# Kernel optimization log

Measured on AMD Instinct MI355X. Metric: run time of the kernel, lower is better.

The kernel has to match this reference:

```python
import jax, jax.numpy as jnp
import numpy as np

B_SZ, SEQ, H, N, NB = 64, 2048, 256, 256, 2
NUM_ITEMS, NC = 200000, 101
EPS = 1e-5


def _ln(x, g, b):
    m = x.mean(-1, keepdims=True)
    v = ((x - m) ** 2).mean(-1, keepdims=True)
    return (x - m) / jnp.sqrt(v + EPS) * g + b


def _s4(u, log_A_real, A_imag, Bp, Cp, Dp, log_step):
    # u: [B,S,H]; diagonal complex S4 recurrence x_{t} = A_bar*x_{t-1} + B_bar u_t
    step = jnp.exp(log_step)                      # [1]
    A = -jnp.exp(log_A_real) + 1j * A_imag        # [N] complex64
    A_bar = jnp.exp(A * step)                     # [N]
    # faithful to torch broadcast (requires N==H): coef scales hidden axis
    B_bar = ((A_bar - 1.0) / A)[None, :] * Bp     # [N,H] complex
    Cc = Cp[..., 0] + 1j * Cp[..., 1]             # [H,N] complex

    def step_fn(x, u_t):                          # x: [B,N] complex, u_t: [B,H]
        x = A_bar[None, :] * x + (u_t.astype(jnp.complex64) @ B_bar.T)
        y = jnp.real(jnp.einsum('hn,bn->bh', Cc, x)) + Dp[None, :] * u_t
        return x, y

    x0 = jnp.zeros((u.shape[0], N), dtype=jnp.complex64)
    _, ys = jax.lax.scan(step_fn, x0, jnp.swapaxes(u, 0, 1))  # ys: [S,B,H]
    return jnp.swapaxes(ys, 0, 1)


def setup_inputs():
    key = jax.random.key(0)
    ks = jax.random.split(key, 16)
    d = {}
    d['input_seqs'] = jax.random.randint(ks[0], (B_SZ, SEQ), 0, NUM_ITEMS + 1)
    d['item_idxs'] = jax.random.randint(ks[1], (B_SZ, NC), 0, NUM_ITEMS + 1)
    d['item_emb'] = jax.random.normal(ks[2], (NUM_ITEMS + 1, H)) * 0.02
    d['pos_emb'] = jax.random.normal(ks[3], (SEQ, H)) * 0.02
    d['ln_g'] = jnp.ones((NB, H)); d['ln_b'] = jnp.zeros((NB, H))
    d['log_A_real'] = jax.random.normal(ks[4], (NB, N))
    d['A_imag'] = jax.random.normal(ks[5], (NB, N))
    d['B_ssm'] = jax.random.normal(ks[6], (NB, N, H))
    d['C_ssm'] = jax.random.normal(ks[7], (NB, H, N, 2))
    d['D_ssm'] = jax.random.normal(ks[8], (NB, H))
    d['log_step'] = jax.random.normal(ks[9], (NB, 1)) * 0.1
    d['W1'] = jax.random.normal(ks[10], (NB, H, H)) / np.sqrt(H).astype(np.float32)
    d['b1'] = jnp.zeros((NB, H))
    d['W2'] = jax.random.normal(ks[11], (NB, H, H)) / np.sqrt(H).astype(np.float32)
    d['b2'] = jnp.zeros((NB, H))
    d['ln_f_g'] = jnp.ones((H,)); d['ln_f_b'] = jnp.zeros((H,))
    return d


def reference(input_seqs, item_idxs, item_emb, pos_emb, ln_g, ln_b,
              log_A_real, A_imag, B_ssm, C_ssm, D_ssm, log_step,
              W1, b1, W2, b2, ln_f_g, ln_f_b):
    mask = (input_seqs != 0).astype(item_emb.dtype)          # [B,S]
    x = item_emb[input_seqs] + pos_emb[None, :, :]           # [B,S,H]
    x = x * mask[..., None]
    for i in range(NB):
        h = _ln(x, ln_g[i], ln_b[i])
        x = x + _s4(h, log_A_real[i], A_imag[i], B_ssm[i], C_ssm[i], D_ssm[i], log_step[i])
        h2 = _ln(x, ln_g[i], ln_b[i])
        x = x + (jax.nn.relu(h2 @ W1[i] + b1[i]) @ W2[i] + b2[i])
        x = x * mask[..., None]
    x = _ln(x, ln_f_g, ln_f_b)
    cand = item_emb[item_idxs]                               # [B,C,H]
    logits = jnp.einsum('bh,bch->bc', x[:, -1], cand)        # [B,C]
    return logits
```

## Files before the change

kernel.cpp:

```cpp
#include <hip/hip_runtime.h>
#include <hip/hip_bf16.h>

#define BSZ 64
#define SEQ 2048
#define HD  256
#define ND  256
#define BS_TOK (BSZ*SEQ)
#define NCAND 101
#define EPS 1e-5f

using bf16 = __hip_bfloat16;
typedef unsigned short u16;
typedef unsigned int   u32;
typedef __attribute__((ext_vector_type(8))) short short8v;
typedef __attribute__((ext_vector_type(4))) float f32x4;

__device__ __forceinline__ float clampf(float v, float c) { return fminf(fmaxf(v, -c), c); }

__device__ __forceinline__ void split_bf(float x, u16& h, u16& l) {
  u32 u = __float_as_uint(x);
  h = (u16)(u >> 16);
  float d = x - __uint_as_float(u & 0xffff0000u);
  l = (u16)(__float_as_uint(d) >> 16);
}
__device__ __forceinline__ float comb_bf(u16 h, u16 l) {
  return __uint_as_float((u32)h << 16) + __uint_as_float((u32)l << 16);
}

__device__ __forceinline__ void async_copy16(const void* g, void* l) {
  __builtin_amdgcn_global_load_lds(
      (const __attribute__((address_space(1))) void*)g,
      (__attribute__((address_space(3))) void*)l, 16, 0, 0);
}


static constexpr size_t MiB = 1024*1024;
static constexpr size_t OFF_X    = 0;
static constexpr size_t OFF_PR   = 128*MiB;
static constexpr size_t OFF_WB   = OFF_PR + 4096;
static constexpr size_t OFF_XLR  = OFF_WB + 4*MiB;
static constexpr size_t OFF_XLI  = OFF_XLR + 65536;
static constexpr size_t OFF_YL   = OFF_XLI + 65536;
static constexpr size_t OFF_XF   = OFF_YL  + 65536;
static constexpr size_t OFF_CH   = 136*MiB;

static constexpr int WB_BB0H = 0,       WB_BB0L = 131072;
static constexpr int WB_BB1H = 262144,  WB_BB1L = 393216;
static constexpr int WB_WSH  = 524288,  WB_WSL  = 655360;
static constexpr int WB_W1H  = 786432,  WB_W1L  = 851968;
static constexpr int WB_W2H  = 917504,  WB_W2L  = 983040;

__global__ __launch_bounds__(256) void pack_k(
    const float* __restrict__ lar, const float* __restrict__ aim, const float* __restrict__ lstep,
    const float* __restrict__ C0, const float* __restrict__ W1, const float* __restrict__ W2,
    const float* __restrict__ Bf,
    float* __restrict__ pr, u16* __restrict__ wb)
{
  int gid = blockIdx.x*256 + threadIdx.x;
  if (gid < 512) {
    int blk = gid >> 8;
    float step = expf(clampf(lstep[blk], 10.f));
    float ar = -expf(clampf(lar[gid], 20.f));
    float ai = aim[gid];
    float er = expf(fminf(ar*step, 0.f));
    pr[gid]       = er * cosf(ai*step);
    pr[512 + gid] = er * sinf(ai*step);
  }
  int r = gid >> 8, c = gid & 255;
  u16 h, l;
#pragma unroll
  for (int blk = 0; blk < 2; ++blk) {
    float step = expf(clampf(lstep[blk], 10.f));
    float ar = -expf(clampf(lar[blk*256 + c], 20.f));
    float ai = aim[blk*256 + c];
    float er  = expf(fminf(ar*step, 0.f));
    float abr = er * cosf(ai*step);
    float abi = er * sinf(ai*step);
    float den = ar*ar + ai*ai;
    float tr = abr - 1.f, ti = abi;
    float cr = (tr*ar + ti*ai) / den;
    float ci = (ti*ar - tr*ai) / den;
    float bv = Bf[blk*65536 + r*256 + c];
    u16* Bh = wb + (blk ? WB_BB1H : WB_BB0H);
    u16* Bl = wb + (blk ? WB_BB1L : WB_BB0L);
    split_bf(cr * bv, h, l); Bh[r*256 + c] = h;         Bl[r*256 + c] = l;
    split_bf(ci * bv, h, l); Bh[(256+r)*256 + c] = h;   Bl[(256+r)*256 + c] = l;
  }
  split_bf( C0[(size_t)(r*256 + c)*2    ], h, l);
  wb[WB_WSH + r*512 + c] = h;        wb[WB_WSL + r*512 + c] = l;
  split_bf(-C0[(size_t)(r*256 + c)*2 + 1], h, l);
  wb[WB_WSH + r*512 + 256 + c] = h;  wb[WB_WSL + r*512 + 256 + c] = l;
  split_bf(W1[c*256 + r], h, l); wb[WB_W1H + r*256 + c] = h; wb[WB_W1L + r*256 + c] = l;
  split_bf(W2[c*256 + r], h, l); wb[WB_W2H + r*256 + c] = h; wb[WB_W2L + r*256 + c] = l;
}

__device__ __forceinline__ void store4_planes(u16* rowp, int lane, int rb7,
                                              float a, float b, float c, float d) {
  int idx = ((lane >> 4) << 7) + (((((lane & 15) >> 1)) ^ rb7) << 3) + ((lane & 1) << 2);
  u16 h0,l0,h1,l1,h2,l2,h3,l3;
  split_bf(a, h0, l0); split_bf(b, h1, l1); split_bf(c, h2, l2); split_bf(d, h3, l3);
  *(uint2*)(rowp + idx)      = make_uint2((u32)h0 | ((u32)h1 << 16), (u32)h2 | ((u32)h3 << 16));
  *(uint2*)(rowp + idx + 64) = make_uint2((u32)l0 | ((u32)l1 << 16), (u32)l2 | ((u32)l3 << 16));
}

__global__ __launch_bounds__(256) void ln_emb_k(
    const int* __restrict__ seqs, const float* __restrict__ iemb,
    const float* __restrict__ pemb,
    const float* __restrict__ g, const float* __restrict__ b,
    float* __restrict__ Xf, u16* __restrict__ OutP, const float* __restrict__ Dv)
{
  int w = threadIdx.x >> 6, lane = threadIdx.x & 63;
  size_t row = (size_t)blockIdx.x * 4 + w;
  int id = seqs[row];
  int pos = (int)(row & (SEQ-1));
  float x[4] = {0.f, 0.f, 0.f, 0.f};
  if (id != 0) {
    float4 ev = ((const float4*)(iemb + (size_t)id*HD))[lane];
    float4 pv = ((const float4*)(pemb + (size_t)pos*HD))[lane];
    x[0] = ev.x + pv.x; x[1] = ev.y + pv.y; x[2] = ev.z + pv.z; x[3] = ev.w + pv.w;
  }
  float s = 0.f, s2 = 0.f;
#pragma unroll
  for (int k = 0; k < 4; ++k) { s += x[k]; s2 += x[k]*x[k]; }
#pragma unroll
  for (int off = 32; off > 0; off >>= 1) { s += __shfl_xor(s, off, 64); s2 += __shfl_xor(s2, off, 64); }
  float m = s * (1.f/256.f);
  float var = fmaxf(s2 * (1.f/256.f) - m*m, 0.f);
  float rinv = rsqrtf(var + EPS);
  int c0 = lane*4;
  float u[4], nx[4];
#pragma unroll
  for (int k = 0; k < 4; ++k) {
    u[k] = (x[k] - m) * rinv * g[c0+k] + b[c0+k];
    nx[k] = x[k] + Dv[c0+k] * u[k];
  }
  store4_planes(OutP + row*512, lane, (int)(row & 7), u[0], u[1], u[2], u[3]);
  ((float4*)(Xf + row*HD))[lane] = make_float4(nx[0], nx[1], nx[2], nx[3]);
}

__global__ __launch_bounds__(256) void ln_rows(
    float* __restrict__ Xf, const float* __restrict__ g, const float* __restrict__ b,
    u16* __restrict__ OutP)
{
  int w = threadIdx.x >> 6, lane = threadIdx.x & 63;
  size_t row = (size_t)blockIdx.x * 4 + w;
  float* xrow = Xf + row*HD;
  float4 xv = ((const float4*)xrow)[lane];
  float x[4] = {xv.x, xv.y, xv.z, xv.w};
  float s = 0.f, s2 = 0.f;
#pragma unroll
  for (int k = 0; k < 4; ++k) { s += x[k]; s2 += x[k]*x[k]; }
#pragma unroll
  for (int off = 32; off > 0; off >>= 1) { s += __shfl_xor(s, off, 64); s2 += __shfl_xor(s2, off, 64); }
  float m = s * (1.f/256.f);
  float var = fmaxf(s2 * (1.f/256.f) - m*m, 0.f);
  float rinv = rsqrtf(var + EPS);
  int c0 = lane*4;
  float u[4];
#pragma unroll
  for (int k = 0; k < 4; ++k) u[k] = (x[k] - m) * rinv * g[c0+k] + b[c0+k];
  store4_planes(OutP + row*512, lane, (int)(row & 7), u[0], u[1], u[2], u[3]);
}

template<int EPI, int CB_N>
__global__ __launch_bounds__(256) void mgemm(
    const u16* __restrict__ A, int ldp,
    const u16* __restrict__ Bh, const u16* __restrict__ Bl, int K, int ldo,
    float* __restrict__ Xf, float* __restrict__ Of, u16* __restrict__ Op,
    const float* __restrict__ bias, const int* __restrict__ ids)
{
  __shared__ __align__(16) u16 As[2][16384];
  const int tid  = threadIdx.x;
  const int lane = tid & 63, wid = tid >> 6;
  const int wr = wid >> 1, wc = wid & 1;
  const int l16 = lane & 15, lhi = lane >> 4;
  int g = blockIdx.x;
  int xx = g & 7, j = g >> 3;
  int cb = j % CB_N, rbk = j / CB_N;
  const int m0 = (rbk*8 + xx) * 128;
  const int n0 = cb*128 + wc*64;
  f32x4 acc[4][4] = {};

  auto stage = [&](int buf, int kb) {
    const int ggo = (kb >> 6) << 7;
#pragma unroll
    for (int i = 0; i < 8; ++i) {
      int q = wid*8 + i;
      int ch = q*64 + lane;
      int rr = ch >> 4, jj = ch & 15;
      const u16* src = A + (size_t)(m0 + rr)*ldp + ggo + jj*8;
      async_copy16(src, &As[buf][q*512]);
    }
  };

  stage(0, 0);
  __syncthreads();
  int cur = 0;
  for (int kb = 0; kb < K; kb += 64) {
    if (kb + 64 < K) stage(cur ^ 1, kb + 64);
#pragma unroll
    for (int kk = 0; kk < 64; kk += 32) {
      short8v ahf[4], alf[4];
      const int c8 = (kk >> 3) + lhi;
#pragma unroll
      for (int rf = 0; rf < 4; ++rf) {
        int r = wr*64 + rf*16 + l16;
        int off = r*128 + ((c8 ^ (r & 7)) << 3);
        ahf[rf] = *(const short8v*)&As[cur][off];
        alf[rf] = *(const short8v*)&As[cur][off + 64];
      }
#pragma unroll
      for (int nf = 0; nf < 4; ++nf) {
        size_t bo = (size_t)(n0 + nf*16 + l16)*K + kb + kk + lhi*8;
        short8v bh = *(const short8v*)(Bh + bo);
        short8v bl = *(const short8v*)(Bl + bo);
#pragma unroll
        for (int rf = 0; rf < 4; ++rf) {
          f32x4 c = acc[rf][nf];
          c = __builtin_amdgcn_mfma_f32_16x16x32_bf16(alf[rf], bh, c, 0, 0, 0);
          c = __builtin_amdgcn_mfma_f32_16x16x32_bf16(ahf[rf], bl, c, 0, 0, 0);
          c = __builtin_amdgcn_mfma_f32_16x16x32_bf16(ahf[rf], bh, c, 0, 0, 0);
          acc[rf][nf] = c;
        }
      }
    }
    __syncthreads();
    cur ^= 1;
  }
#pragma unroll
  for (int rf = 0; rf < 4; ++rf) {
#pragma unroll
    for (int jj = 0; jj < 4; ++jj) {
      int row = m0 + wr*64 + rf*16 + lhi*4 + jj;
      int rb7 = row & 7;
      int idv = 0;
      if (EPI == 3) idv = ids[row];
#pragma unroll
      for (int nf = 0; nf < 4; ++nf) {
        int col = n0 + nf*16 + l16;
        float v = acc[rf][nf][jj];
        if (EPI == 0) {
          Of[(size_t)row*ldo + col] = v;
        } else if (EPI == 2) {
          float t = fmaxf(v + bias[col], 0.f);
          u16 hh, ll; split_bf(t, hh, ll);
          size_t base = (size_t)row*ldo + ((col >> 6) << 7)
                      + ((((col >> 3) & 7) ^ rb7) << 3) + (col & 7);
          Op[base] = hh; Op[base + 64] = ll;
        } else if (EPI == 3) {
          size_t idx = (size_t)row*ldo + col;
          float t = Xf[idx] + v + bias[col];
          Xf[idx] = (idv != 0) ? t : 0.f;
        } else {
          size_t idx = (size_t)row*ldo + col;
          Xf[idx] = Xf[idx] + v;
        }
      }
    }
  }
}

template<bool STORE>
__global__ __launch_bounds__(1024) void pscan_k(
    float* __restrict__ Sb,
    const float* __restrict__ arp, const float* __restrict__ aip,
    float* __restrict__ xlast_r, float* __restrict__ xlast_i)
{
  __shared__ float sR[16][64], sI[16][64];
  int lane = threadIdx.x & 63;
  int w = threadIdx.x >> 6;
  int b = blockIdx.x >> 2;
  int sg = blockIdx.x & 3;
  int n = (sg << 6) | lane;
  float Ar = arp[n], Ai = aip[n];
  float p128r = Ar, p128i = Ai;
#pragma unroll
  for (int i = 0; i < 7; ++i) {
    float nr = p128r*p128r - p128i*p128i, ni = 2.f*p128r*p128i;
    p128r = nr; p128i = ni;
  }
  const int t0 = w*128;
  const float* sp = Sb + ((size_t)b*SEQ + t0)*512 + n;
  u16* qp16 = (u16*)(Sb + (size_t)b*SEQ*512);
  const int sgo = sg << 7;
  const int lo3 = lane & 7, lh3 = lane >> 3;

  float xr = 0.f, xi = 0.f;
#pragma unroll 4
  for (int t = 0; t < 128; ++t) {
    float sr = sp[0], si = sp[256];
    float nxr = Ar*xr - Ai*xi + sr;
    float nxi = Ar*xi + Ai*xr + si;
    xr = nxr; xi = nxi;
    if (STORE) {
      int tt = t0 + t;
      size_t si2 = (size_t)tt*1024 + sgo + (((lh3 ^ (tt & 7))) << 3) + lo3;
      u16 hh, ll;
      split_bf(xr, hh, ll); qp16[si2] = hh;       qp16[si2 + 64]  = ll;
      split_bf(xi, hh, ll); qp16[si2 + 512] = hh; qp16[si2 + 576] = ll;
    }
    sp += 512;
  }

  sR[w][lane] = xr; sI[w][lane] = xi;
  __syncthreads();
  float er = 0.f, ei = 0.f;
  for (int q = 0; q < w; ++q) {
    float tr = p128r*er - p128i*ei + sR[q][lane];
    float ti = p128r*ei + p128i*er + sI[q][lane];
    er = tr; ei = ti;
  }

  if (!STORE) {
    if (w == 15) {
      float fr = p128r*er - p128i*ei + sR[15][lane];
      float fi = p128r*ei + p128i*er + sI[15][lane];
      xlast_r[b*ND + n] = fr; xlast_i[b*ND + n] = fi;
    }
    return;
  }

  if (w == 0) return;
  float cr = Ar*er - Ai*ei, ci = Ar*ei + Ai*er;
#pragma unroll 4
  for (int t = 0; t < 128; ++t) {
    int tt = t0 + t;
    size_t si2 = (size_t)tt*1024 + sgo + (((lh3 ^ (tt & 7))) << 3) + lo3;
    float vr = comb_bf(qp16[si2],       qp16[si2 + 64])  + cr;
    float vi = comb_bf(qp16[si2 + 512], qp16[si2 + 576]) + ci;
    u16 hh, ll;
    split_bf(vr, hh, ll); qp16[si2] = hh;       qp16[si2 + 64]  = ll;
    split_bf(vi, hh, ll); qp16[si2 + 512] = hh; qp16[si2 + 576] = ll;
    float nr = Ar*cr - Ai*ci, ni = Ar*ci + Ai*cr;
    cr = nr; ci = ni;
  }
}

__global__ __launch_bounds__(256) void ylast_k(
    const float* __restrict__ xr, const float* __restrict__ xi,
    const float* __restrict__ C1, const float* __restrict__ D1,
    const u16* __restrict__ U,
    const float* __restrict__ Xf, int b0, float* __restrict__ ylr)
{
  int bl = blockIdx.x, h = threadIdx.x;
  __shared__ float sxr[256], sxi[256];
  sxr[h] = xr[bl*256 + h]; sxi[h] = xi[bl*256 + h];
  __syncthreads();
  float acc = 0.f;
  for (int n = 0; n < 256; ++n) {
    acc += C1[(size_t)(h*256 + n)*2] * sxr[n] - C1[(size_t)(h*256 + n)*2 + 1] * sxi[n];
  }
  size_t lrow = (size_t)bl*SEQ + SEQ - 1;
  size_t ub = lrow*512 + ((h >> 6) << 7) + ((((h >> 3) & 7) ^ 7) << 3) + (h & 7);
  float uval = comb_bf(U[ub], U[ub + 64]);
  size_t gidx = ((size_t)(b0 + bl)*SEQ + SEQ - 1)*HD + h;
  ylr[(b0 + bl)*256 + h] = Xf[gidx] + acc + D1[h] * uval;
}

__device__ __forceinline__ float block_sum256(float v, volatile float* red) {
#pragma unroll
  for (int off = 32; off > 0; off >>= 1) v += __shfl_xor(v, off, 64);
  int w = threadIdx.x >> 6;
  __syncthreads();
  if ((threadIdx.x & 63) == 0) red[w] = v;
  __syncthreads();
  return red[0] + red[1] + red[2] + red[3];
}

__global__ __launch_bounds__(256) void tail_k(
    const float* __restrict__ ylr, const float* __restrict__ g1, const float* __restrict__ bb1,
    const float* __restrict__ W1p, const float* __restrict__ b1p,
    const float* __restrict__ W2p, const float* __restrict__ b2p,
    const float* __restrict__ fg, const float* __restrict__ fb,
    const int* __restrict__ seqs, float* __restrict__ xfin)
{
  __shared__ float sh[256];
  __shared__ float red[4];
  int b = blockIdx.x, h = threadIdx.x;
  float x = ylr[b*256 + h];
  float m = block_sum256(x, red) * (1.f/256.f);
  float d = x - m;
  float var = fmaxf(block_sum256(d*d, red) * (1.f/256.f), 0.f);
  float h2 = d * rsqrtf(var + EPS) * g1[h] + bb1[h];
  __syncthreads();
  sh[h] = h2;
  __syncthreads();
  float acc = 0.f;
  for (int k = 0; k < 256; ++k) acc += sh[k] * W1p[k*256 + h];
  float f = fmaxf(acc + b1p[h], 0.f);
  __syncthreads();
  sh[h] = f;
  __syncthreads();
  acc = 0.f;
  for (int k = 0; k < 256; ++k) acc += sh[k] * W2p[k*256 + h];
  float x2 = x + acc + b2p[h];
  if (seqs[b*SEQ + SEQ - 1] == 0) x2 = 0.f;
  float m2 = block_sum256(x2, red) * (1.f/256.f);
  float d2 = x2 - m2;
  float v2 = fmaxf(block_sum256(d2*d2, red) * (1.f/256.f), 0.f);
  xfin[b*256 + h] = d2 * rsqrtf(v2 + EPS) * fg[h] + fb[h];
}

__global__ __launch_bounds__(256) void logits_k(
    const float* __restrict__ xfin, const int* __restrict__ cand,
    const float* __restrict__ iemb, float* __restrict__ out)
{
  int gid = blockIdx.x*4 + (threadIdx.x >> 6);
  if (gid >= BSZ*NCAND) return;
  int lane = threadIdx.x & 63;
  int b = gid / NCAND;
  int id = cand[gid];
  const float* e  = iemb + (size_t)id*HD;
  const float* xv = xfin + b*256;
  float acc = 0.f;
#pragma unroll
  for (int k = 0; k < 4; ++k) acc += xv[lane*4 + k] * e[lane*4 + k];
#pragma unroll
  for (int off = 32; off > 0; off >>= 1) acc += __shfl_xor(acc, off, 64);
  if (lane == 0) out[gid] = acc;
}

extern "C" void kernel_launch(void* const* d_in, const int* in_sizes, int n_in,
                              void* d_out, int out_size, void* d_ws, size_t ws_size,
                              hipStream_t stream)
{
  const int*   seqs  = (const int*)d_in[0];
  const int*   cand  = (const int*)d_in[1];
  const float* iemb  = (const float*)d_in[2];
  const float* pemb  = (const float*)d_in[3];
  const float* ln_g  = (const float*)d_in[4];
  const float* ln_b  = (const float*)d_in[5];
  const float* lar   = (const float*)d_in[6];
  const float* aim   = (const float*)d_in[7];
  const float* Bssm  = (const float*)d_in[8];
  const float* Cssm  = (const float*)d_in[9];
  const float* Dssm  = (const float*)d_in[10];
  const float* lstep = (const float*)d_in[11];
  const float* W1    = (const float*)d_in[12];
  const float* b1    = (const float*)d_in[13];
  const float* W2    = (const float*)d_in[14];
  const float* b2    = (const float*)d_in[15];
  const float* lnfg  = (const float*)d_in[16];
  const float* lnfb  = (const float*)d_in[17];

  char* ws = (char*)d_ws;
  float* Xf   = (float*)(ws + OFF_X);
  float* pr   = (float*)(ws + OFF_PR);
  u16*   wb   = (u16*)  (ws + OFF_WB);
  float* xlr  = (float*)(ws + OFF_XLR);
  float* xli  = (float*)(ws + OFF_XLI);
  float* ylr  = (float*)(ws + OFF_YL);
  float* xfin = (float*)(ws + OFF_XF);

  int CB = 64;
  while (CB > 1 && (OFF_CH + (size_t)6*CB*MiB) > ws_size) CB >>= 1;
  u16*   HbP = (u16*)(ws + OFF_CH);
  float* SbC = (float*)(ws + OFF_CH + (size_t)2*CB*MiB);

  pack_k<<<256, 256, 0, stream>>>(lar, aim, lstep, Cssm, W1, W2, Bssm, pr, wb);

  const int rows = CB*SEQ;
  const int rb   = rows / 128;
  for (int b0 = 0; b0 < BSZ; b0 += CB) {
    float* XfC = Xf + (size_t)b0*SEQ*HD;
    const int* seqC = seqs + (size_t)b0*SEQ;

    ln_emb_k<<<rows/4, 256, 0, stream>>>(seqC, iemb, pemb, ln_g, ln_b, XfC, HbP, Dssm);
    mgemm<0,4><<<4*rb, 256, 0, stream>>>(HbP, 512, wb + WB_BB0H, wb + WB_BB0L, 256, 512,
                                         nullptr, SbC, nullptr, nullptr, nullptr);
    pscan_k<true><<<CB*4, 1024, 0, stream>>>(SbC, pr, pr+512, nullptr, nullptr);
    mgemm<4,2><<<2*rb, 256, 0, stream>>>((u16*)SbC, 1024, wb + WB_WSH, wb + WB_WSL, 512, 256,
                                         XfC, nullptr, nullptr, nullptr, nullptr);
    ln_rows<<<rows/4, 256, 0, stream>>>(XfC, ln_g, ln_b, HbP);
    mgemm<2,2><<<2*rb, 256, 0, stream>>>(HbP, 512, wb + WB_W1H, wb + WB_W1L, 256, 512,
                                         nullptr, nullptr, (u16*)SbC, b1, nullptr);
    mgemm<3,2><<<2*rb, 256, 0, stream>>>((u16*)SbC, 512, wb + WB_W2H, wb + WB_W2L, 256, 256,
                                         XfC, nullptr, nullptr, b2, seqC);
    ln_rows<<<rows/4, 256, 0, stream>>>(XfC, ln_g + 256, ln_b + 256, HbP);
    mgemm<0,4><<<4*rb, 256, 0, stream>>>(HbP, 512, wb + WB_BB1H, wb + WB_BB1L, 256, 512,
                                         nullptr, SbC, nullptr, nullptr, nullptr);
    pscan_k<false><<<CB*4, 1024, 0, stream>>>(SbC, pr+256, pr+768, xlr + b0*256, xli + b0*256);
    ylast_k<<<CB, 256, 0, stream>>>(xlr + b0*256, xli + b0*256, Cssm + 2*65536, Dssm + 256,
                                    HbP, Xf, b0, ylr);
  }

  tail_k<<<BSZ, 256, 0, stream>>>(ylr, ln_g + 256, ln_b + 256, W1 + 65536, b1 + 256,
                                  W2 + 65536, b2 + 256, lnfg, lnfb, seqs, xfin);
  logits_k<<<(BSZ*NCAND + 3)/4, 256, 0, stream>>>(xfin, cand, iemb, (float*)d_out);
}
```

Before: 1.706 ms.

## Fuse FFN up and down projections into one kernel keeping hidden in LDS

```diff
diff --git a/kernel.cpp b/kernel.cpp
--- a/kernel.cpp
+++ b/kernel.cpp
@@ -260,6 +260,120 @@
   }
 }
 
+__global__ __launch_bounds__(512) void ffn_k(
+    const u16* __restrict__ A,
+    const u16* __restrict__ W1h, const u16* __restrict__ W1l,
+    const u16* __restrict__ W2h, const u16* __restrict__ W2l,
+    const float* __restrict__ b1p, const float* __restrict__ b2p,
+    float* __restrict__ Xf, const int* __restrict__ ids)
+{
+  __shared__ __align__(16) u16 As[16384];
+  __shared__ __align__(16) u16 Ts[16384];
+  const int tid = threadIdx.x;
+  const int lane = tid & 63, w = tid >> 6;
+  const int l16 = lane & 15, lhi = lane >> 4;
+  const int m0 = blockIdx.x * 32;
+
+#pragma unroll
+  for (int i = 0; i < 4; ++i) {
+    int rr = i*8 + w;
+    async_copy16(A + (size_t)(m0 + rr)*512 + lane*8, &As[rr*512]);
+  }
+  __syncthreads();
+
+  f32x4 acc[2][2] = {};
+#pragma unroll
+  for (int ks = 0; ks < 8; ++ks) {
+    const int kk = ks*32;
+    const int c8g = (kk >> 3) + lhi;
+    const int gg = c8g >> 3, cg = c8g & 7;
+    short8v ahf[2], alf[2];
+#pragma unroll
+    for (int rf = 0; rf < 2; ++rf) {
+      int r = rf*16 + l16;
+      int off = r*512 + gg*128 + ((cg ^ (r & 7)) << 3);
+      ahf[rf] = *(const short8v*)&As[off];
+      alf[rf] = *(const short8v*)&As[off + 64];
+    }
+#pragma unroll
+    for (int cf = 0; cf < 2; ++cf) {
+      size_t bo = (size_t)(w*32 + cf*16 + l16)*256 + kk + lhi*8;
+      short8v bh = *(const short8v*)(W1h + bo);
+      short8v bl = *(const short8v*)(W1l + bo);
+#pragma unroll
+      for (int rf = 0; rf < 2; ++rf) {
+        f32x4 c = acc[rf][cf];
+        c = __builtin_amdgcn_mfma_f32_16x16x32_bf16(alf[rf], bh, c, 0, 0, 0);
+        c = __builtin_amdgcn_mfma_f32_16x16x32_bf16(ahf[rf], bl, c, 0, 0, 0);
+        c = __builtin_amdgcn_mfma_f32_16x16x32_bf16(ahf[rf], bh, c, 0, 0, 0);
+        acc[rf][cf] = c;
+      }
+    }
+  }
+#pragma unroll
+  for (int rf = 0; rf < 2; ++rf) {
+#pragma unroll
+    for (int jj = 0; jj < 4; ++jj) {
+      int row = rf*16 + lhi*4 + jj;
+      int rb7 = row & 7;
+#pragma unroll
+      for (int cf = 0; cf < 2; ++cf) {
+        int col = w*32 + cf*16 + l16;
+        float t = fmaxf(acc[rf][cf][jj] + b1p[col], 0.f);
+        u16 hh, ll; split_bf(t, hh, ll);
+        int base = row*512 + ((col >> 6) << 7) + ((((col >> 3) & 7) ^ rb7) << 3) + (col & 7);
+        Ts[base] = hh; Ts[base + 64] = ll;
+      }
+    }
+  }
+  __syncthreads();
+
+  f32x4 acc2[2][2] = {};
+#pragma unroll
+  for (int ks = 0; ks < 8; ++ks) {
+    const int kk = ks*32;
+    const int c8g = (kk >> 3) + lhi;
+    const int gg = c8g >> 3, cg = c8g & 7;
+    short8v ahf[2], alf[2];
+#pragma unroll
+    for (int rf = 0; rf < 2; ++rf) {
+      int r = rf*16 + l16;
+      int off = r*512 + gg*128 + ((cg ^ (r & 7)) << 3);
+      ahf[rf] = *(const short8v*)&Ts[off];
+      alf[rf] = *(const short8v*)&Ts[off + 64];
+    }
+#pragma unroll
+    for (int cf = 0; cf < 2; ++cf) {
+      size_t bo = (size_t)(w*32 + cf*16 + l16)*256 + kk + lhi*8;
+      short8v bh = *(const short8v*)(W2h + bo);
+      short8v bl = *(const short8v*)(W2l + bo);
+#pragma unroll
+      for (int rf = 0; rf < 2; ++rf) {
+        f32x4 c = acc2[rf][cf];
+        c = __builtin_amdgcn_mfma_f32_16x16x32_bf16(alf[rf], bh, c, 0, 0, 0);
+        c = __builtin_amdgcn_mfma_f32_16x16x32_bf16(ahf[rf], bl, c, 0, 0, 0);
+        c = __builtin_amdgcn_mfma_f32_16x16x32_bf16(ahf[rf], bh, c, 0, 0, 0);
+        acc2[rf][cf] = c;
+      }
+    }
+  }
+#pragma unroll
+  for (int rf = 0; rf < 2; ++rf) {
+#pragma unroll
+    for (int jj = 0; jj < 4; ++jj) {
+      int row = m0 + rf*16 + lhi*4 + jj;
+      int idv = ids[row];
+#pragma unroll
+      for (int cf = 0; cf < 2; ++cf) {
+        int col = w*32 + cf*16 + l16;
+        size_t idx = (size_t)row*HD + col;
+        float t = Xf[idx] + acc2[rf][cf][jj] + b2p[col];
+        Xf[idx] = (idv != 0) ? t : 0.f;
+      }
+    }
+  }
+}
+
 template<bool STORE>
 __global__ __launch_bounds__(1024) void pscan_k(
     float* __restrict__ Sb,
@@ -472,10 +586,8 @@
     mgemm<4,2><<<2*rb, 256, 0, stream>>>((u16*)SbC, 1024, wb + WB_WSH, wb + WB_WSL, 512, 256,
                                          XfC, nullptr, nullptr, nullptr, nullptr);
     ln_rows<<<rows/4, 256, 0, stream>>>(XfC, ln_g, ln_b, HbP);
-    mgemm<2,2><<<2*rb, 256, 0, stream>>>(HbP, 512, wb + WB_W1H, wb + WB_W1L, 256, 512,
-                                         nullptr, nullptr, (u16*)SbC, b1, nullptr);
-    mgemm<3,2><<<2*rb, 256, 0, stream>>>((u16*)SbC, 512, wb + WB_W2H, wb + WB_W2L, 256, 256,
-                                         XfC, nullptr, nullptr, b2, seqC);
+    ffn_k<<<rows/32, 512, 0, stream>>>(HbP, wb + WB_W1H, wb + WB_W1L, wb + WB_W2H, wb + WB_W2L,
+                                       b1, b2, XfC, seqC);
     ln_rows<<<rows/4, 256, 0, stream>>>(XfC, ln_g + 256, ln_b + 256, HbP);
     mgemm<0,4><<<4*rb, 256, 0, stream>>>(HbP, 512, wb + WB_BB1H, wb + WB_BB1L, 256, 512,
                                          nullptr, SbC, nullptr, nullptr, nullptr);
```

Result: faster. 1.646 ms (-3.5%).
